# Optimization experiments

Measured on AMD Instinct MI355X. Metric: run time of the kernel, lower is better.

## Reference

```python
import jax, jax.numpy as jnp
import numpy as np

B, N, C, H = 8192, 17, 512, 8
HD = C // H  # head dim = 64


def setup_inputs() -> dict:
    key = jax.random.key(0)
    ks = jax.random.split(key, 7)
    s = 0.02
    return {
        "x": jax.random.normal(ks[0], (B, N, C), dtype=jnp.float32),
        "W_qkv": jax.random.normal(ks[1], (C, 3 * C), dtype=jnp.float32) * s,
        "b_qkv": jax.random.normal(ks[2], (3 * C,), dtype=jnp.float32) * s,
        "outer": jax.random.normal(ks[3], (H, N, N), dtype=jnp.float32) * s,
        "alpha": jnp.ones((1,), dtype=jnp.float32),
        "W_proj": jax.random.normal(ks[4], (C, C), dtype=jnp.float32) * s,
        "b_proj": jax.random.normal(ks[5], (C,), dtype=jnp.float32) * s,
    }


def reference(x, W_qkv, b_qkv, outer, alpha, W_proj, b_proj):
    scale = HD ** -0.5
    qkv = x @ W_qkv + b_qkv                       # [B,N,3C]
    qkv = qkv.reshape(B, N, 3, H, HD)
    q = jnp.transpose(qkv[:, :, 0], (0, 2, 1, 3))  # [B,H,N,HD]
    k = jnp.transpose(qkv[:, :, 1], (0, 2, 1, 3))
    v = jnp.transpose(qkv[:, :, 2], (0, 2, 1, 3))
    # comb=False path: (q @ k^T + alpha * outer) * scale, softmax, @ v
    logits = (jnp.einsum('bhnd,bhmd->bhnm', q, k) + alpha * outer[None]) * scale
    attn = jax.nn.softmax(logits, axis=-1)        # [B,H,N,N]
    out = jnp.einsum('bhnm,bhmd->bhnd', attn, v)  # [B,H,N,HD]
    out = jnp.transpose(out, (0, 2, 1, 3)).reshape(B, N, C)
    return out @ W_proj + b_proj
```

## Files before the change

### kernel.cpp

```cpp
#include <hip/hip_runtime.h>
#include <stdint.h>


typedef __attribute__((ext_vector_type(4))) float f32x4;
typedef _Float16 f16x8 __attribute__((ext_vector_type(8)));
typedef _Float16 f16x4 __attribute__((ext_vector_type(4)));
typedef _Float16 f16x2 __attribute__((ext_vector_type(2)));

__device__ __forceinline__ unsigned short f2h(float f) {
  return __builtin_bit_cast(unsigned short, (_Float16)f);
}
__device__ __forceinline__ float h2f(unsigned short h) {
  return (float)__builtin_bit_cast(_Float16, h);
}
__device__ __forceinline__ float fdot2u(uint32_t a, uint32_t b, float c) {
  return __builtin_amdgcn_fdot2(__builtin_bit_cast(f16x2, a),
                                __builtin_bit_cast(f16x2, b), c, false);
}

#define GLOAD_LDS16(gptr, lptr)                                          \
  __builtin_amdgcn_global_load_lds(                                      \
      (__attribute__((address_space(1))) void*)(gptr),                   \
      (__attribute__((address_space(3))) void*)(lptr), 16, 0, 0)

#define VMCNT(n) asm volatile("s_waitcnt vmcnt(" #n ")" ::: "memory")

__device__ __forceinline__ f32x4 mfma16(f16x8 a, f16x8 b, f32x4 c) {
  return __builtin_amdgcn_mfma_f32_16x16x32_f16(a, b, c, 0, 0, 0);
}
__device__ __forceinline__ f32x4 mfma16k16(f16x4 a, f16x4 b, f32x4 c) {
  return __builtin_amdgcn_mfma_f32_16x16x16f16(a, b, c, 0, 0, 0);
}

__global__ __launch_bounds__(256) void k_cvt(const float* __restrict__ in,
                                             unsigned short* __restrict__ out,
                                             long n4) {
  long i = (long)blockIdx.x * 256 + threadIdx.x;
  if (i >= n4) return;
  float4 a = reinterpret_cast<const float4*>(in)[i];
  ushort4 o;
  o.x = f2h(a.x); o.y = f2h(a.y); o.z = f2h(a.z); o.w = f2h(a.w);
  reinterpret_cast<ushort4*>(out)[i] = o;
}

template <bool PERM>
__global__ __launch_bounds__(256) void k_cvt_t(const float* __restrict__ W,
                                               unsigned short* __restrict__ Wt,
                                               int K, int Norig) {
  int i = blockIdx.x * 256 + threadIdx.x;
  if (i >= K * Norig) return;
  int np = i / K, k = i - np * K;
  int n = np;
  if (PERM) {
    int h = np / 192, rem = np - h * 192;
    int t = rem >> 6, d = rem & 63;
    n = t * 512 + h * 64 + d;
  }
  Wt[i] = f2h(W[(size_t)k * Norig + n]);
}

__global__ __launch_bounds__(256) void k_permb(const float* __restrict__ b,
                                               float* __restrict__ bqp) {
  int np = blockIdx.x * 256 + threadIdx.x;
  if (np >= 1536) return;
  int h = np / 192, rem = np - h * 192;
  int t = rem >> 6, d = rem & 63;
  bqp[np] = b[t * 512 + h * 64 + d];
}

__global__ __launch_bounds__(512, 4) void k_fused(
    const unsigned short* __restrict__ A,
    const unsigned short* __restrict__ Bt,
    const float* __restrict__ bqp,
    const float* __restrict__ outer,
    const float* __restrict__ alpha_p,
    unsigned short* __restrict__ ao) {
  __shared__ __align__(16) unsigned short smem[40960];

  const int tid = threadIdx.x;
  const int w = tid >> 6, lane = tid & 63;
  const int wm = w >> 2, wn = w & 3;
  const int lr = lane & 15, lk = lane >> 4;

  const int bid = (blockIdx.x & 7) * ((int)gridDim.x >> 3) + (blockIdx.x >> 3);
  const int mt = bid >> 3, h = bid & 7;
  const int batch0 = mt * 7;
  const int brow = batch0 * 17;
  const int bcol = h * 192;

  const int rsl = lane >> 2;
  const int swcol = ((lane & 3) ^ ((lane >> 3) & 3)) << 3;
  const bool cw3 = (w < 4);

  f32x4 acc[4][3];
#pragma unroll
  for (int m = 0; m < 4; m++)
#pragma unroll
    for (int n = 0; n < 3; n++) acc[m][n] = f32x4{0.f, 0.f, 0.f, 0.f};

  auto STAGE1 = [&](int t, int s) {
    unsigned short* dst = smem + (t & 3) * 10240 + s * 512;
    const unsigned short* src;
    if (s < 8) {
      int gr = brow + s * 16 + rsl;
      if (gr > 139263) gr = 139263;
      src = A + (size_t)gr * 512 + t * 32 + swcol;
    } else {
      src = Bt + (size_t)(bcol + (s - 8) * 16 + rsl) * 512 + t * 32 + swcol;
    }
    GLOAD_LDS16(src, dst);
  };
  auto STAGE = [&](int t) {
    STAGE1(t, w);
    STAGE1(t, w + 8);
    if (cw3) STAGE1(t, w + 16);
  };

  STAGE(0); STAGE(1); STAGE(2);
  if (cw3) { VMCNT(6); } else { VMCNT(4); }
  __builtin_amdgcn_s_barrier();

  const int gx = (lk ^ ((lr >> 1) & 3)) << 3;
  for (int t = 0; t < 16; ++t) {
    if (t + 3 < 16) STAGE(t + 3);
    const unsigned short* bufp = smem + (t & 3) * 10240;
    const unsigned short* sa = bufp + (wm * 64 + lr) * 32 + gx;
    const unsigned short* sb = bufp + 4096 + (wn * 48 + lr) * 32 + gx;
    f16x8 a0 = *(const f16x8*)(sa);
    f16x8 a1 = *(const f16x8*)(sa + 512);
    f16x8 a2 = *(const f16x8*)(sa + 1024);
    f16x8 a3 = *(const f16x8*)(sa + 1536);
    f16x8 b0 = *(const f16x8*)(sb);
    f16x8 b1 = *(const f16x8*)(sb + 512);
    f16x8 b2 = *(const f16x8*)(sb + 1024);
    acc[0][0] = mfma16(a0, b0, acc[0][0]);
    acc[0][1] = mfma16(a0, b1, acc[0][1]);
    acc[0][2] = mfma16(a0, b2, acc[0][2]);
    acc[1][0] = mfma16(a1, b0, acc[1][0]);
    acc[1][1] = mfma16(a1, b1, acc[1][1]);
    acc[1][2] = mfma16(a1, b2, acc[1][2]);
    acc[2][0] = mfma16(a2, b0, acc[2][0]);
    acc[2][1] = mfma16(a2, b1, acc[2][1]);
    acc[2][2] = mfma16(a2, b2, acc[2][2]);
    acc[3][0] = mfma16(a3, b0, acc[3][0]);
    acc[3][1] = mfma16(a3, b1, acc[3][1]);
    acc[3][2] = mfma16(a3, b2, acc[3][2]);
    if (t < 13) {
      if (cw3) { VMCNT(6); } else { VMCNT(4); }
    } else if (t == 13) {
      if (cw3) { VMCNT(3); } else { VMCNT(2); }
    } else if (t == 14) {
      VMCNT(0);
    }
    __builtin_amdgcn_s_barrier();
  }

  unsigned short* SQ = smem;
  unsigned short* VT = smem + 17408;
  unsigned short* PL = smem + 29696;
  float* SE = (float*)(smem + 32768);

  {
    const int er0 = wm * 64 + (lane >> 4) * 4;
    const int ec0 = wn * 48 + lr;
#pragma unroll
    for (int nf = 0; nf < 3; ++nf) {
      const int col = ec0 + nf * 16;
      const float bv = bqp[bcol + col];
#pragma unroll
      for (int mf = 0; mf < 4; ++mf) {
        const int t0 = er0 + mf * 16;
        float v0 = acc[mf][nf][0] + bv, v1 = acc[mf][nf][1] + bv;
        float v2 = acc[mf][nf][2] + bv, v3 = acc[mf][nf][3] + bv;
        if (col < 128) {
          SQ[(t0 + 0) * 136 + col] = f2h(v0);
          SQ[(t0 + 1) * 136 + col] = f2h(v1);
          SQ[(t0 + 2) * 136 + col] = f2h(v2);
          SQ[(t0 + 3) * 136 + col] = f2h(v3);
        } else {
          const int d = col - 128;
#pragma unroll
          for (int rr = 0; rr < 4; ++rr) {
            const int tt = t0 + rr;
            const int bb = tt / 17, tl = tt - bb * 17;
            float vv = (rr == 0 ? v0 : rr == 1 ? v1 : rr == 2 ? v2 : v3);
            if (bb < 7) VT[bb * 1536 + d * 24 + tl] = f2h(vv);
          }
        }
      }
    }
  }
  __syncthreads();

  const int nb = min(7, 8192 - batch0);
  if (w < nb) {
    const float alpha = alpha_p[0];
    const int base = w * 17;
    unsigned short* PLw = PL + w * 384;
    unsigned short* VTw = VT + w * 1536;
    float* SEw = SE + w * 34;

    f32x4 sAcc = f32x4{0.f, 0.f, 0.f, 0.f};
#pragma unroll
    for (int kk = 0; kk < 2; ++kk) {
      f16x8 qa = *(const f16x8*)(SQ + (base + lr) * 136 + kk * 32 + lk * 8);
      f16x8 kb = *(const f16x8*)(SQ + (base + lr) * 136 + 64 + kk * 32 + lk * 8);
      sAcc = mfma16(qa, kb, sAcc);
    }

    if (lane < 33) {
      const int r_ = (lane < 16) ? lane : 16;
      const int m_ = (lane < 16) ? 16 : lane - 16;
      const uint4* qr = (const uint4*)(SQ + (base + r_) * 136);
      const uint4* kr = (const uint4*)(SQ + (base + m_) * 136 + 64);
      float dt = 0.f;
#pragma unroll
      for (int c = 0; c < 8; ++c) {
        uint4 qa = qr[c], ka = kr[c];
        dt = fdot2u(qa.x, ka.x, dt);
        dt = fdot2u(qa.y, ka.y, dt);
        dt = fdot2u(qa.z, ka.z, dt);
        dt = fdot2u(qa.w, ka.w, dt);
      }
      float sv = (dt + alpha * outer[h * 289 + r_ * 17 + m_]) * 0.125f;
      SEw[(lane < 16) ? lane : (17 + m_)] = sv;
    }
    __builtin_amdgcn_wave_barrier();
    asm volatile("" ::: "memory");

    const int g4 = (lane >> 4) * 4;
    float sp[4], rmax[4], p[4], pe[4], rsum[4], inv[4];
#pragma unroll
    for (int j = 0; j < 4; ++j) {
      sp[j] = (sAcc[j] + alpha * outer[h * 289 + (g4 + j) * 17 + lr]) * 0.125f;
      rmax[j] = sp[j];
    }
#pragma unroll
    for (int d = 1; d < 16; d <<= 1)
#pragma unroll
      for (int j = 0; j < 4; ++j)
        rmax[j] = fmaxf(rmax[j], __shfl_xor(rmax[j], d));
#pragma unroll
    for (int j = 0; j < 4; ++j) {
      float ec = SEw[g4 + j];
      rmax[j] = fmaxf(rmax[j], ec);
      p[j] = __expf(sp[j] - rmax[j]);
      pe[j] = __expf(ec - rmax[j]);
      rsum[j] = p[j];
    }
#pragma unroll
    for (int d = 1; d < 16; d <<= 1)
#pragma unroll
      for (int j = 0; j < 4; ++j) rsum[j] += __shfl_xor(rsum[j], d);
#pragma unroll
    for (int j = 0; j < 4; ++j) {
      rsum[j] += pe[j];
      inv[j] = 1.f / rsum[j];
      PLw[(g4 + j) * 24 + lr] = f2h(p[j]);
    }
    __builtin_amdgcn_wave_barrier();
    asm volatile("" ::: "memory");

    f16x4 pa = *(const f16x4*)(PLw + lr * 24 + lk * 4);
    f32x4 o[4];
    float v16[4];
#pragma unroll
    for (int nf = 0; nf < 4; ++nf) {
      f16x4 vb = *(const f16x4*)(VTw + (nf * 16 + lr) * 24 + lk * 4);
      o[nf] = mfma16k16(pa, vb, f32x4{0.f, 0.f, 0.f, 0.f});
      v16[nf] = h2f(VTw[(nf * 16 + lr) * 24 + 16]);
    }
    const size_t gr0 = (size_t)(brow + base) * 512 + h * 64;
#pragma unroll
    for (int nf = 0; nf < 4; ++nf)
#pragma unroll
      for (int j = 0; j < 4; ++j)
        ao[gr0 + (size_t)(g4 + j) * 512 + nf * 16 + lr] =
            f2h((o[nf][j] + pe[j] * v16[nf]) * inv[j]);

    {
      float mx16 = -1e30f;
#pragma unroll 1
      for (int m = 0; m < 17; ++m) mx16 = fmaxf(mx16, SEw[17 + m]);
      float o16 = 0.f, s16 = 0.f;
#pragma unroll 1
      for (int m = 0; m < 17; ++m) {
        float pm = __expf(SEw[17 + m] - mx16);
        s16 += pm;
        o16 += pm * h2f(VTw[lane * 24 + m]);
      }
      ao[gr0 + (size_t)16 * 512 + lane] = f2h(o16 / s16);
    }
  }
}

__global__ __launch_bounds__(512, 4) void k_proj(
    const unsigned short* __restrict__ A,
    const unsigned short* __restrict__ Bt,
    const float* __restrict__ bias,
    float* __restrict__ C) {
  __shared__ __align__(16) unsigned short smem[32768];

  const int tid = threadIdx.x;
  const int w = tid >> 6, lane = tid & 63;
  const int wm = w >> 2, wn = w & 3;
  const int lr = lane & 15, lk = lane >> 4;

  const int bid = (blockIdx.x & 7) * ((int)gridDim.x >> 3) + (blockIdx.x >> 3);
  const int brow = (bid >> 2) << 7;
  const int bcol = (bid & 3) << 7;

  const int rsl = lane >> 2;
  const int swcol = ((lane & 3) ^ ((lane >> 3) & 3)) << 3;

  f32x4 acc[4][2];
#pragma unroll
  for (int m = 0; m < 4; m++)
#pragma unroll
    for (int n = 0; n < 2; n++) acc[m][n] = f32x4{0.f, 0.f, 0.f, 0.f};

  auto STAGE1 = [&](int t, int s) {
    unsigned short* dst = smem + (t & 3) * 8192 + s * 512;
    const unsigned short* src =
        (s < 8) ? A + (size_t)(brow + s * 16 + rsl) * 512 + t * 32 + swcol
                : Bt + (size_t)(bcol + (s - 8) * 16 + rsl) * 512 + t * 32 + swcol;
    GLOAD_LDS16(src, dst);
  };
  auto STAGE = [&](int t) {
    STAGE1(t, w);
    STAGE1(t, w + 8);
  };

  STAGE(0); STAGE(1); STAGE(2);
  VMCNT(4);
  __builtin_amdgcn_s_barrier();

  const int gx = (lk ^ ((lr >> 1) & 3)) << 3;
  for (int t = 0; t < 16; ++t) {
    if (t + 3 < 16) STAGE(t + 3);
    const unsigned short* bufp = smem + (t & 3) * 8192;
    const unsigned short* sa = bufp + (wm * 64 + lr) * 32 + gx;
    const unsigned short* sb = bufp + 4096 + (wn * 32 + lr) * 32 + gx;
    f16x8 a0 = *(const f16x8*)(sa);
    f16x8 a1 = *(const f16x8*)(sa + 512);
    f16x8 a2 = *(const f16x8*)(sa + 1024);
    f16x8 a3 = *(const f16x8*)(sa + 1536);
    f16x8 b0 = *(const f16x8*)(sb);
    f16x8 b1 = *(const f16x8*)(sb + 512);
    acc[0][0] = mfma16(a0, b0, acc[0][0]);
    acc[0][1] = mfma16(a0, b1, acc[0][1]);
    acc[1][0] = mfma16(a1, b0, acc[1][0]);
    acc[1][1] = mfma16(a1, b1, acc[1][1]);
    acc[2][0] = mfma16(a2, b0, acc[2][0]);
    acc[2][1] = mfma16(a2, b1, acc[2][1]);
    acc[3][0] = mfma16(a3, b0, acc[3][0]);
    acc[3][1] = mfma16(a3, b1, acc[3][1]);
    if (t < 13) {
      VMCNT(4);
    } else if (t == 13) {
      VMCNT(2);
    } else if (t == 14) {
      VMCNT(0);
    }
    __builtin_amdgcn_s_barrier();
  }

  const int orow = brow + wm * 64 + (lane >> 4) * 4;
  const int ocol0 = bcol + wn * 32 + lr;
#pragma unroll
  for (int n = 0; n < 2; n++) {
    const int col = ocol0 + n * 16;
    const float bv = bias[col];
#pragma unroll
    for (int m = 0; m < 4; m++) {
      const int row = orow + m * 16;
#pragma unroll
      for (int r = 0; r < 4; r++)
        C[(size_t)(row + r) * 512 + col] = acc[m][n][r] + bv;
    }
  }
}

extern "C" void kernel_launch(void* const* d_in, const int* in_sizes, int n_in,
                              void* d_out, int out_size, void* d_ws,
                              size_t ws_size, hipStream_t stream) {
  const float* x      = (const float*)d_in[0];
  const float* W_qkv  = (const float*)d_in[1];
  const float* b_qkv  = (const float*)d_in[2];
  const float* outer  = (const float*)d_in[3];
  const float* alpha  = (const float*)d_in[4];
  const float* W_proj = (const float*)d_in[5];
  const float* b_proj = (const float*)d_in[6];

  char* ws = (char*)d_ws;
  unsigned short* xb  = (unsigned short*)(ws);
  unsigned short* ao  = (unsigned short*)(ws + 142606336);
  unsigned short* wqt = (unsigned short*)(ws + 285212672);
  unsigned short* wpt = (unsigned short*)(ws + 286785536);
  float*          bqp = (float*)(ws + 287309824);

  k_cvt<<<dim3(69632), dim3(256), 0, stream>>>(x, xb, 17825792L);
  k_cvt_t<true><<<dim3(3072), dim3(256), 0, stream>>>(W_qkv, wqt, 512, 1536);
  k_cvt_t<false><<<dim3(1024), dim3(256), 0, stream>>>(W_proj, wpt, 512, 512);
  k_permb<<<dim3(6), dim3(256), 0, stream>>>(b_qkv, bqp);

  k_fused<<<dim3(9368), dim3(512), 0, stream>>>(xb, wqt, bqp, outer, alpha, ao);

  k_proj<<<dim3(4352), dim3(512), 0, stream>>>(ao, wpt, b_proj, (float*)d_out);
}
```

Baseline: 607.8 us.

## Double block tiles to 1024 threads in fused QKV-attention and projection kernels

The fused QKV+attention kernel now uses 1024-thread blocks covering 15 batches (255 rows) per tile instead of 7, and the projection GEMM moves from 128x128 to 256x256 tiles with 16 waves and 4x4 MFMA fragments per wave. Larger tiles are meant to raise reuse of the staged weight tiles and cut redundant global loads of W and A. In exchange, LDS use per block grows to about 128 KB, which limits occupancy to one block per CU. The grid is also smaller, so wave-quantization tail effects may increase.

```diff
diff --git a/kernel.cpp b/kernel.cpp
--- a/kernel.cpp
+++ b/kernel.cpp
@@ -68,29 +68,31 @@
   bqp[np] = b[t * 512 + h * 64 + d];
 }
 
-__global__ __launch_bounds__(512, 4) void k_fused(
+#define FBUFS 14336
+
+__global__ __launch_bounds__(1024, 4) void k_fused(
     const unsigned short* __restrict__ A,
     const unsigned short* __restrict__ Bt,
     const float* __restrict__ bqp,
     const float* __restrict__ outer,
     const float* __restrict__ alpha_p,
     unsigned short* __restrict__ ao) {
-  __shared__ __align__(16) unsigned short smem[40960];
+  __shared__ __align__(16) unsigned short smem[64640];
 
   const int tid = threadIdx.x;
   const int w = tid >> 6, lane = tid & 63;
   const int wm = w >> 2, wn = w & 3;
   const int lr = lane & 15, lk = lane >> 4;
 
-  const int bid = (blockIdx.x & 7) * ((int)gridDim.x >> 3) + (blockIdx.x >> 3);
-  const int mt = bid >> 3, h = bid & 7;
-  const int batch0 = mt * 7;
+  const int g = (blockIdx.x & 7) * 547 + (blockIdx.x >> 3);
+  const int mt = g >> 3, h = g & 7;
+  const int batch0 = mt * 15;
   const int brow = batch0 * 17;
   const int bcol = h * 192;
 
   const int rsl = lane >> 2;
   const int swcol = ((lane & 3) ^ ((lane >> 3) & 3)) << 3;
-  const bool cw3 = (w < 4);
+  const bool cw2 = (w < 12);
 
   f32x4 acc[4][3];
 #pragma unroll
@@ -99,33 +101,32 @@
     for (int n = 0; n < 3; n++) acc[m][n] = f32x4{0.f, 0.f, 0.f, 0.f};
 
   auto STAGE1 = [&](int t, int s) {
-    unsigned short* dst = smem + (t & 3) * 10240 + s * 512;
+    unsigned short* dst = smem + (t & 3) * FBUFS + s * 512;
     const unsigned short* src;
-    if (s < 8) {
+    if (s < 16) {
       int gr = brow + s * 16 + rsl;
       if (gr > 139263) gr = 139263;
       src = A + (size_t)gr * 512 + t * 32 + swcol;
     } else {
-      src = Bt + (size_t)(bcol + (s - 8) * 16 + rsl) * 512 + t * 32 + swcol;
+      src = Bt + (size_t)(bcol + (s - 16) * 16 + rsl) * 512 + t * 32 + swcol;
     }
     GLOAD_LDS16(src, dst);
   };
   auto STAGE = [&](int t) {
     STAGE1(t, w);
-    STAGE1(t, w + 8);
-    if (cw3) STAGE1(t, w + 16);
+    if (cw2) STAGE1(t, 16 + w);
   };
 
   STAGE(0); STAGE(1); STAGE(2);
-  if (cw3) { VMCNT(6); } else { VMCNT(4); }
+  if (cw2) { VMCNT(4); } else { VMCNT(2); }
   __builtin_amdgcn_s_barrier();
 
   const int gx = (lk ^ ((lr >> 1) & 3)) << 3;
   for (int t = 0; t < 16; ++t) {
     if (t + 3 < 16) STAGE(t + 3);
-    const unsigned short* bufp = smem + (t & 3) * 10240;
+    const unsigned short* bufp = smem + (t & 3) * FBUFS;
     const unsigned short* sa = bufp + (wm * 64 + lr) * 32 + gx;
-    const unsigned short* sb = bufp + 4096 + (wn * 48 + lr) * 32 + gx;
+    const unsigned short* sb = bufp + 8192 + (wn * 48 + lr) * 32 + gx;
     f16x8 a0 = *(const f16x8*)(sa);
     f16x8 a1 = *(const f16x8*)(sa + 512);
     f16x8 a2 = *(const f16x8*)(sa + 1024);
@@ -146,9 +147,9 @@
     acc[3][1] = mfma16(a3, b1, acc[3][1]);
     acc[3][2] = mfma16(a3, b2, acc[3][2]);
     if (t < 13) {
-      if (cw3) { VMCNT(6); } else { VMCNT(4); }
+      if (cw2) { VMCNT(4); } else { VMCNT(2); }
     } else if (t == 13) {
-      if (cw3) { VMCNT(3); } else { VMCNT(2); }
+      if (cw2) { VMCNT(2); } else { VMCNT(1); }
     } else if (t == 14) {
       VMCNT(0);
     }
@@ -156,9 +157,9 @@
   }
 
   unsigned short* SQ = smem;
-  unsigned short* VT = smem + 17408;
-  unsigned short* PL = smem + 29696;
-  float* SE = (float*)(smem + 32768);
+  unsigned short* VT = smem + 34816;
+  unsigned short* PL = smem + 57856;
+  float* SE = (float*)(smem + 63616);
 
   {
     const int er0 = wm * 64 + (lane >> 4) * 4;
@@ -184,7 +185,7 @@
             const int tt = t0 + rr;
             const int bb = tt / 17, tl = tt - bb * 17;
             float vv = (rr == 0 ? v0 : rr == 1 ? v1 : rr == 2 ? v2 : v3);
-            if (bb < 7) VT[bb * 1536 + d * 24 + tl] = f2h(vv);
+            if (bb < 15) VT[bb * 1536 + d * 24 + tl] = f2h(vv);
           }
         }
       }
@@ -192,7 +193,7 @@
   }
   __syncthreads();
 
-  const int nb = min(7, 8192 - batch0);
+  const int nb = min(15, 8192 - batch0);
   if (w < nb) {
     const float alpha = alpha_p[0];
     const int base = w * 17;
@@ -294,41 +295,43 @@
   }
 }
 
-__global__ __launch_bounds__(512, 4) void k_proj(
+#define PBUFS 16384
+
+__global__ __launch_bounds__(1024, 4) void k_proj(
     const unsigned short* __restrict__ A,
     const unsigned short* __restrict__ Bt,
     const float* __restrict__ bias,
     float* __restrict__ C) {
-  __shared__ __align__(16) unsigned short smem[32768];
+  __shared__ __align__(16) unsigned short smem[65536];
 
   const int tid = threadIdx.x;
   const int w = tid >> 6, lane = tid & 63;
   const int wm = w >> 2, wn = w & 3;
   const int lr = lane & 15, lk = lane >> 4;
 
-  const int bid = (blockIdx.x & 7) * ((int)gridDim.x >> 3) + (blockIdx.x >> 3);
-  const int brow = (bid >> 2) << 7;
-  const int bcol = (bid & 3) << 7;
+  const int g = (blockIdx.x & 7) * 136 + (blockIdx.x >> 3);
+  const int brow = (g >> 1) << 8;
+  const int bcol = (g & 1) << 8;
 
   const int rsl = lane >> 2;
   const int swcol = ((lane & 3) ^ ((lane >> 3) & 3)) << 3;
 
-  f32x4 acc[4][2];
+  f32x4 acc[4][4];
 #pragma unroll
   for (int m = 0; m < 4; m++)
 #pragma unroll
-    for (int n = 0; n < 2; n++) acc[m][n] = f32x4{0.f, 0.f, 0.f, 0.f};
+    for (int n = 0; n < 4; n++) acc[m][n] = f32x4{0.f, 0.f, 0.f, 0.f};
 
   auto STAGE1 = [&](int t, int s) {
-    unsigned short* dst = smem + (t & 3) * 8192 + s * 512;
+    unsigned short* dst = smem + (t & 3) * PBUFS + s * 512;
     const unsigned short* src =
-        (s < 8) ? A + (size_t)(brow + s * 16 + rsl) * 512 + t * 32 + swcol
-                : Bt + (size_t)(bcol + (s - 8) * 16 + rsl) * 512 + t * 32 + swcol;
+        (s < 16) ? A + (size_t)(brow + s * 16 + rsl) * 512 + t * 32 + swcol
+                 : Bt + (size_t)(bcol + (s - 16) * 16 + rsl) * 512 + t * 32 + swcol;
     GLOAD_LDS16(src, dst);
   };
   auto STAGE = [&](int t) {
     STAGE1(t, w);
-    STAGE1(t, w + 8);
+    STAGE1(t, 16 + w);
   };
 
   STAGE(0); STAGE(1); STAGE(2);
@@ -338,23 +341,19 @@
   const int gx = (lk ^ ((lr >> 1) & 3)) << 3;
   for (int t = 0; t < 16; ++t) {
     if (t + 3 < 16) STAGE(t + 3);
-    const unsigned short* bufp = smem + (t & 3) * 8192;
+    const unsigned short* bufp = smem + (t & 3) * PBUFS;
     const unsigned short* sa = bufp + (wm * 64 + lr) * 32 + gx;
-    const unsigned short* sb = bufp + 4096 + (wn * 32 + lr) * 32 + gx;
-    f16x8 a0 = *(const f16x8*)(sa);
-    f16x8 a1 = *(const f16x8*)(sa + 512);
-    f16x8 a2 = *(const f16x8*)(sa + 1024);
-    f16x8 a3 = *(const f16x8*)(sa + 1536);
-    f16x8 b0 = *(const f16x8*)(sb);
-    f16x8 b1 = *(const f16x8*)(sb + 512);
-    acc[0][0] = mfma16(a0, b0, acc[0][0]);
-    acc[0][1] = mfma16(a0, b1, acc[0][1]);
-    acc[1][0] = mfma16(a1, b0, acc[1][0]);
-    acc[1][1] = mfma16(a1, b1, acc[1][1]);
-    acc[2][0] = mfma16(a2, b0, acc[2][0]);
-    acc[2][1] = mfma16(a2, b1, acc[2][1]);
-    acc[3][0] = mfma16(a3, b0, acc[3][0]);
-    acc[3][1] = mfma16(a3, b1, acc[3][1]);
+    const unsigned short* sb = bufp + 8192 + (wn * 64 + lr) * 32 + gx;
+    f16x8 av[4], bv[4];
+#pragma unroll
+    for (int m = 0; m < 4; m++) av[m] = *(const f16x8*)(sa + m * 512);
+#pragma unroll
+    for (int n = 0; n < 4; n++) bv[n] = *(const f16x8*)(sb + n * 512);
+#pragma unroll
+    for (int m = 0; m < 4; m++)
+#pragma unroll
+      for (int n = 0; n < 4; n++)
+        acc[m][n] = mfma16(av[m], bv[n], acc[m][n]);
     if (t < 13) {
       VMCNT(4);
     } else if (t == 13) {
@@ -366,9 +365,9 @@
   }
 
   const int orow = brow + wm * 64 + (lane >> 4) * 4;
-  const int ocol0 = bcol + wn * 32 + lr;
-#pragma unroll
-  for (int n = 0; n < 2; n++) {
+  const int ocol0 = bcol + wn * 64 + lr;
+#pragma unroll
+  for (int n = 0; n < 4; n++) {
     const int col = ocol0 + n * 16;
     const float bv = bias[col];
 #pragma unroll
@@ -404,7 +403,7 @@
   k_cvt_t<false><<<dim3(1024), dim3(256), 0, stream>>>(W_proj, wpt, 512, 512);
   k_permb<<<dim3(6), dim3(256), 0, stream>>>(b_qkv, bqp);
 
-  k_fused<<<dim3(9368), dim3(512), 0, stream>>>(xb, wqt, bqp, outer, alpha, ao);
-
-  k_proj<<<dim3(4352), dim3(512), 0, stream>>>(ao, wpt, b_proj, (float*)d_out);
-}
+  k_fused<<<dim3(4376), dim3(1024), 0, stream>>>(xb, wqt, bqp, outer, alpha, ao);
+
+  k_proj<<<dim3(1088), dim3(1024), 0, stream>>>(ao, wpt, b_proj, (float*)d_out);
+}
```

New measurement: 616.0 us. About the same (+1.4%).
